# Performance work log

Hardware: AMD Instinct MI355X
Metric: run time of the kernel (lower is better)

Reference implementation:

```python
import jax, jax.numpy as jnp
import numpy as np

V, N, D, H, C = 3, 4096, 512, 128, 5  # views, nodes, in_dim, hidden, classes
NEG = -9.0e15   # mask value from original code (-9000000000000000.0)
NEG_SLOPE = 0.25


def _leaky(x, slope):
    return jnp.where(x >= 0, x, slope * x)


def setup_inputs() -> dict:
    key = jax.random.key(0)
    ks = jax.random.split(key, 24)
    g = lambda i, shape, s=0.05: (jax.random.normal(ks[i], shape, dtype=jnp.float32) * s)
    return {
        "data": jax.random.normal(ks[0], (V, N, D), dtype=jnp.float32),
        "adj": jax.random.randint(ks[1], (V, N, N), 0, 2, dtype=jnp.int32),
        "gac_w": g(2, (V, D, H)), "gac_b": g(3, (V, H)),
        "a1": g(4, (V, H)), "a2": g(5, (V, H)),
        "mlp_w": g(6, (V, D, H)), "mlp_b": g(7, (V, H)),
        "q_w": g(8, (V, H, H)), "q_b": g(9, (V, H)),
        "k_w": g(10, (V, H, H)), "k_b": g(11, (V, H)),
        "v_w": g(12, (V, H, H)), "v_b": g(13, (V, H)),
        "fc_w": g(14, (V, H, H)), "fc_b": g(15, (V, H)),
        "conf_w": g(16, (V, H, 1)), "conf_b": g(17, (V, 1)),
        "mm_w": g(18, (V * H, C)), "mm_b": g(19, (C,)),
    }


def reference(data, adj, gac_w, gac_b, a1, a2, mlp_w, mlp_b,
              q_w, q_b, k_w, k_b, v_w, v_b, fc_w, fc_b,
              conf_w, conf_b, mm_w, mm_b):
    # --- GraphAttentionConv (per view, vectorized over v) ---
    h = jnp.einsum('vnd,vdh->vnh', data, gac_w)               # spmm(input, W)
    e1 = jnp.einsum('vnh,vh->vn', h, a1)                      # h @ a1
    e2 = jnp.einsum('vnh,vh->vn', h, a2)                      # h @ a2
    e = _leaky(e1[:, :, None] + e2[:, None, :], NEG_SLOPE)    # [V,N,N] broadcast-add
    e = jnp.where(adj > 0, e, NEG)                            # mask by dense adjacency
    att = jax.nn.softmax(e, axis=-1)                          # row softmax
    feat = jnp.einsum('vnm,vmh->vnh', att, h) + gac_b[:, None, :]
    feat = _leaky(feat, NEG_SLOPE)                            # F.leaky_relu(GAC out, 0.25)
    # residual MLP branch
    feat = feat + jnp.einsum('vnd,vdh->vnh', data, mlp_w) + mlp_b[:, None, :]

    # --- StructureGuidedFeatureEnhancement (n_heads=1): per-node HxH attention ---
    Q = jnp.einsum('vnh,vho->vno', feat, q_w) + q_b[:, None, :]
    K = jnp.einsum('vnh,vho->vno', feat, k_w) + k_b[:, None, :]
    Vv = jnp.einsum('vnh,vho->vno', feat, v_w) + v_b[:, None, :]
    scale = jnp.sqrt(jnp.asarray(H, jnp.float32))
    A = Q[:, :, :, None] * K[:, :, None, :] / scale           # [V,N,H,H] outer product
    A = jax.nn.softmax(A, axis=-1)
    agg = jnp.einsum('vnio,vno->vni', A, Vv)                  # attention @ V
    agg = jnp.einsum('vnh,vho->vno', agg, fc_w) + fc_b[:, None, :]
    feat = jax.nn.relu(agg)

    # --- TCP confidence gating ---
    conf = jnp.einsum('vnh,vho->vno', feat, conf_w) + conf_b[:, None, :]  # [V,N,1]
    feat = feat * conf

    # --- concat views along feature dim, final classifier ---
    mm = jnp.transpose(feat, (1, 0, 2)).reshape(N, V * H)     # [N, V*H]
    return mm @ mm_w + mm_b                                   # MMlogit [N, C]
```

## Files before the change

### kernel.cpp

```cpp
#include <hip/hip_runtime.h>
#include <hip/hip_bf16.h>

#define V 3
#define N 4096
#define D 512
#define H 128
#define C 5

typedef short short8 __attribute__((ext_vector_type(8)));
typedef float floatx4 __attribute__((ext_vector_type(4)));

__device__ __forceinline__ unsigned short f2bf(float f){
  __hip_bfloat16 h = __float2bfloat16(f);
  return *reinterpret_cast<unsigned short*>(&h);
}

#define TN1 16
__global__ __launch_bounds__(256) void k1_gemm(
    const float* __restrict__ data,
    const float* __restrict__ gac_w,
    const float* __restrict__ mlp_w,
    const float* __restrict__ a1, const float* __restrict__ a2,
    unsigned short* __restrict__ hT, float* __restrict__ mlp_out,
    float* __restrict__ e1, float* __restrict__ e2)
{
  const int v = blockIdx.y;
  const int n0 = blockIdx.x * TN1;
  const int t = threadIdx.x;
  const int half = t >> 7, tt = t & 127;
  __shared__ float ds[D][20];
  __shared__ float epart[2][2][TN1];
  float* comb = &ds[0][0];
  const float* dp = data + ((size_t)v*N + n0)*D;
  for (int j = t; j < TN1*D; j += 256){
    int r = j >> 9, d = j & (D-1);
    ds[d][r] = dp[(size_t)r*D + d];
  }
  __syncthreads();
  float ag[TN1], am[TN1];
  #pragma unroll
  for (int r=0;r<TN1;r++){ ag[r]=0.f; am[r]=0.f; }
  const int d0 = half*256;
  const float* gw = gac_w + (size_t)v*D*H + tt;
  const float* mw = mlp_w + (size_t)v*D*H + tt;
  for (int d=d0; d<d0+256; d++){
    float wg = gw[(size_t)d*H];
    float wm = mw[(size_t)d*H];
    const float4* p = (const float4*)&ds[d][0];
    float4 x0=p[0], x1=p[1], x2=p[2], x3=p[3];
    float xv[16] = {x0.x,x0.y,x0.z,x0.w, x1.x,x1.y,x1.z,x1.w,
                    x2.x,x2.y,x2.z,x2.w, x3.x,x3.y,x3.z,x3.w};
    #pragma unroll
    for (int r=0;r<TN1;r++){
      ag[r] = fmaf(xv[r], wg, ag[r]);
      am[r] = fmaf(xv[r], wm, am[r]);
    }
  }
  __syncthreads();
  if (half == 1){
    #pragma unroll
    for (int r=0;r<TN1;r++){
      comb[r*H + tt]          = ag[r];
      comb[TN1*H + r*H + tt]  = am[r];
    }
  }
  __syncthreads();
  if (half == 0){
    float* mp = mlp_out + ((size_t)v*N + n0)*H + tt;
    unsigned short pk[TN1];
    const float a1v = a1[v*H + tt], a2v = a2[v*H + tt];
    #pragma unroll
    for (int r=0;r<TN1;r++){
      ag[r] += comb[r*H + tt];
      am[r] += comb[TN1*H + r*H + tt];
      mp[(size_t)r*H] = am[r];
      pk[r] = f2bf(ag[r]);
    }
    uint4* hp = (uint4*)(hT + ((size_t)v*H + tt)*N + n0);
    hp[0] = *(uint4*)&pk[0];
    hp[1] = *(uint4*)&pk[8];
    #pragma unroll
    for (int r=0;r<TN1;r++){
      float s1 = ag[r]*a1v, s2 = ag[r]*a2v;
      #pragma unroll
      for (int o=32;o>0;o>>=1){ s1 += __shfl_down(s1,o); s2 += __shfl_down(s2,o); }
      if ((tt&63)==0){ epart[0][tt>>6][r]=s1; epart[1][tt>>6][r]=s2; }
    }
  }
  __syncthreads();
  if (t < TN1)            e1[(size_t)v*N + n0 + t]        = epart[0][0][t]    + epart[0][1][t];
  else if (t < 2*TN1)     e2[(size_t)v*N + n0 + (t-TN1)]  = epart[1][0][t-TN1]+ epart[1][1][t-TN1];
}

#define KC 128
__global__ __launch_bounds__(512) void k2_attn(
    const unsigned short* __restrict__ hT, const int* __restrict__ adj,
    const float* __restrict__ e1g, const float* __restrict__ e2g,
    const float* __restrict__ mlp_out,
    const float* __restrict__ gac_b, const float* __restrict__ mlp_b,
    float* __restrict__ feat)
{
  const int v = blockIdx.y;
  const int n0 = blockIdx.x * 16;
  const int t = threadIdx.x;
  const int w = t >> 6, lane = t & 63;
  __shared__ unsigned short Afrag[4][64][8];
  __shared__ float pden_l[8][16];

  const int pr = t & 15, sm = t >> 4;
  const int p_ks   = sm >> 3;
  const int p_lane = pr + 16*((sm>>1)&3);
  const int p_j0   = 4*(sm&1);
  const float e1r = e1g[(size_t)v*N + n0 + pr];
  const int* aprow = adj + ((size_t)v*N + n0 + pr)*N;
  float psum = 0.f;

  const int col = w*16 + (lane & 15);
  const unsigned short* bcol = hT + ((size_t)v*H + col)*N + ((lane>>4)*8);
  floatx4 acc = {0.f, 0.f, 0.f, 0.f};

  for (int m0 = 0; m0 < N; m0 += KC){
    const float4 e2v = *(const float4*)(e2g + (size_t)v*N + m0 + 4*sm);
    const int4  av  = *(const int4*)(aprow + m0 + 4*sm);
    float e2a[4] = {e2v.x, e2v.y, e2v.z, e2v.w};
    int   aa[4]  = {av.x, av.y, av.z, av.w};
    unsigned int pk[2];
    unsigned short us[4];
    #pragma unroll
    for (int jj=0;jj<4;jj++){
      float x = e1r + e2a[jj];
      x = (x >= 0.f) ? x : 0.25f*x;
      float wv = (aa[jj] > 0) ? __expf(x) : 0.f;
      psum += wv;
      us[jj] = f2bf(wv);
    }
    pk[0] = (unsigned int)us[0] | ((unsigned int)us[1] << 16);
    pk[1] = (unsigned int)us[2] | ((unsigned int)us[3] << 16);
    *(uint2*)&Afrag[p_ks][p_lane][p_j0] = make_uint2(pk[0], pk[1]);
    __syncthreads();
    #pragma unroll
    for (int ks=0; ks<4; ks++){
      short8 a8 = *(const short8*)&Afrag[ks][lane][0];
      short8 b8 = *(const short8*)(bcol + m0 + ks*32);
      acc = __builtin_amdgcn_mfma_f32_16x16x32_bf16(a8, b8, acc, 0, 0, 0);
    }
    __syncthreads();
  }
  psum += __shfl_down(psum, 32);
  psum += __shfl_down(psum, 16);
  if (lane < 16) pden_l[w][lane] = psum;
  __syncthreads();
  const float gb = gac_b[v*H + col];
  const float mb = mlp_b[v*H + col];
  #pragma unroll
  for (int reg=0; reg<4; reg++){
    const int row = (lane>>4)*4 + reg;
    float den = 0.f;
    #pragma unroll
    for (int k=0;k<8;k++) den += pden_l[k][row];
    float x = acc[reg]/den + gb;
    x = (x >= 0.f) ? x : 0.25f*x;
    const size_t idx = ((size_t)v*N + n0 + row)*H + col;
    feat[idx] = x + mlp_out[idx] + mb;
  }
}

#define TN3 8
__global__ __launch_bounds__(128) void k3_sgfe(
    const float* __restrict__ feat,
    const float* __restrict__ qw, const float* __restrict__ qb,
    const float* __restrict__ kw, const float* __restrict__ kb,
    const float* __restrict__ vw, const float* __restrict__ vb,
    const float* __restrict__ fcw, const float* __restrict__ fcb,
    const float* __restrict__ confw, const float* __restrict__ confb,
    float* __restrict__ feat2)
{
  const int v = blockIdx.y;
  const int n0 = blockIdx.x * TN3;
  const int t = threadIdx.x;
  const int W = t >> 6, lane = t & 63;
  __shared__ float fsT[H][12];
  __shared__ float Qs[TN3][H];
  __shared__ float2 KVs[TN3][H];
  __shared__ float As2T[H][12];
  __shared__ float rbuf2[TN3][2];
  const float* fp = feat + ((size_t)v*N + n0)*H + t;
  #pragma unroll
  for (int r=0;r<TN3;r++) fsT[t][r] = fp[(size_t)r*H];
  __syncthreads();
  const float* qwp = qw + (size_t)v*H*H + t;
  const float* kwp = kw + (size_t)v*H*H + t;
  const float* vwp = vw + (size_t)v*H*H + t;
  float Qr[TN3], Kr[TN3], Vr[TN3];
  {
    const float qbv = qb[v*H+t], kbv = kb[v*H+t], vbv = vb[v*H+t];
    #pragma unroll
    for (int r=0;r<TN3;r++){ Qr[r]=qbv; Kr[r]=kbv; Vr[r]=vbv; }
  }
  for (int i=0;i<H;i++){
    float wq = qwp[(size_t)i*H];
    float wk = kwp[(size_t)i*H];
    float wv = vwp[(size_t)i*H];
    float4 f0 = *(const float4*)&fsT[i][0];
    float4 f1 = *(const float4*)&fsT[i][4];
    float fv[8] = {f0.x,f0.y,f0.z,f0.w, f1.x,f1.y,f1.z,f1.w};
    #pragma unroll
    for (int r=0;r<TN3;r++){
      Qr[r] = fmaf(fv[r], wq, Qr[r]);
      Kr[r] = fmaf(fv[r], wk, Kr[r]);
      Vr[r] = fmaf(fv[r], wv, Vr[r]);
    }
  }
  #pragma unroll
  for (int r=0;r<TN3;r++){
    Qs[r][t] = Qr[r];
    KVs[r][t] = make_float2(Kr[r], Vr[r]);
  }
  __syncthreads();
  const float invs = 0.08838834764831845f;
  #pragma unroll
  for (int p=0;p<4;p++){
    const int r = 2*p + W;
    const float qa = Qs[r][lane]   * invs;
    const float qb2 = Qs[r][lane+64] * invs;
    float sA=0.f, aA=0.f, sB=0.f, aB=0.f;
    const float4* kvp = (const float4*)&KVs[r][0];
    #pragma unroll 4
    for (int oo=0; oo<H/2; oo++){
      float4 kv2 = kvp[oo];
      float eA0 = __expf(qa*kv2.x);  sA += eA0; aA = fmaf(eA0, kv2.y, aA);
      float eA1 = __expf(qa*kv2.z);  sA += eA1; aA = fmaf(eA1, kv2.w, aA);
      float eB0 = __expf(qb2*kv2.x); sB += eB0; aB = fmaf(eB0, kv2.y, aB);
      float eB1 = __expf(qb2*kv2.z); sB += eB1; aB = fmaf(eB1, kv2.w, aB);
    }
    As2T[lane][r]    = aA/sA;
    As2T[lane+64][r] = aB/sB;
  }
  __syncthreads();
  const float* fcwp = fcw + (size_t)v*H*H + t;
  const float fcbv = fcb[v*H+t];
  float g[TN3];
  #pragma unroll
  for (int r=0;r<TN3;r++) g[r] = fcbv;
  for (int i=0;i<H;i++){
    float fw = fcwp[(size_t)i*H];
    float4 a0 = *(const float4*)&As2T[i][0];
    float4 a1v = *(const float4*)&As2T[i][4];
    g[0] = fmaf(a0.x, fw, g[0]);  g[1] = fmaf(a0.y, fw, g[1]);
    g[2] = fmaf(a0.z, fw, g[2]);  g[3] = fmaf(a0.w, fw, g[3]);
    g[4] = fmaf(a1v.x, fw, g[4]); g[5] = fmaf(a1v.y, fw, g[5]);
    g[6] = fmaf(a1v.z, fw, g[6]); g[7] = fmaf(a1v.w, fw, g[7]);
  }
  const float cwv = confw[v*H+t];
  const float cbv = confb[v];
  #pragma unroll
  for (int r=0;r<TN3;r++){
    g[r] = fmaxf(g[r], 0.f);
    float psm = g[r]*cwv;
    #pragma unroll
    for (int o=32;o>0;o>>=1) psm += __shfl_down(psm,o);
    if (lane==0) rbuf2[r][W] = psm;
  }
  __syncthreads();
  #pragma unroll
  for (int r=0;r<TN3;r++){
    const float conf = rbuf2[r][0] + rbuf2[r][1] + cbv;
    feat2[((size_t)v*N + n0 + r)*H + t] = g[r]*conf;
  }
}

__global__ __launch_bounds__(64) void k4_cls(
    const float* __restrict__ feat2,
    const float* __restrict__ mm_w, const float* __restrict__ mm_b,
    float* __restrict__ out)
{
  const int n = blockIdx.x, t = threadIdx.x;
  float a[C] = {0,0,0,0,0};
  for (int j=t; j<V*H; j+=64){
    int vv = j >> 7, hh = j & (H-1);
    float f = feat2[((size_t)vv*N + n)*H + hh];
    #pragma unroll
    for (int c=0;c<C;c++) a[c] = fmaf(f, mm_w[j*C+c], a[c]);
  }
  #pragma unroll
  for (int c=0;c<C;c++){
    #pragma unroll
    for (int o=32;o>0;o>>=1) a[c] += __shfl_down(a[c],o);
  }
  if (t==0){
    #pragma unroll
    for (int c=0;c<C;c++) out[(size_t)n*C+c] = a[c] + mm_b[c];
  }
}

extern "C" void kernel_launch(void* const* d_in, const int* in_sizes, int n_in,
                              void* d_out, int out_size, void* d_ws, size_t ws_size,
                              hipStream_t stream)
{
  (void)in_sizes; (void)n_in; (void)out_size; (void)ws_size;
  const float* data  = (const float*)d_in[0];
  const int*   adj   = (const int*)d_in[1];
  const float* gac_w = (const float*)d_in[2];
  const float* gac_b = (const float*)d_in[3];
  const float* a1    = (const float*)d_in[4];
  const float* a2    = (const float*)d_in[5];
  const float* mlp_w = (const float*)d_in[6];
  const float* mlp_b = (const float*)d_in[7];
  const float* q_w   = (const float*)d_in[8];
  const float* q_b   = (const float*)d_in[9];
  const float* k_w   = (const float*)d_in[10];
  const float* k_b   = (const float*)d_in[11];
  const float* v_w   = (const float*)d_in[12];
  const float* v_b   = (const float*)d_in[13];
  const float* fc_w  = (const float*)d_in[14];
  const float* fc_b  = (const float*)d_in[15];
  const float* cw    = (const float*)d_in[16];
  const float* cb    = (const float*)d_in[17];
  const float* mm_w  = (const float*)d_in[18];
  const float* mm_b  = (const float*)d_in[19];

  float* ws = (float*)d_ws;
  const size_t VNH = (size_t)V*N*H;
  float* mlp   = ws;
  float* feat  = ws + VNH;
  float* feat2 = ws + 2*VNH;
  float* e1    = ws + 3*VNH;
  float* e2    = e1 + (size_t)V*N;
  unsigned short* hT = (unsigned short*)(e2 + (size_t)V*N);

  k1_gemm<<<dim3(N/TN1, V), 256, 0, stream>>>(data, gac_w, mlp_w, a1, a2,
                                              hT, mlp, e1, e2);
  k2_attn<<<dim3(N/16, V),  512, 0, stream>>>(hT, adj, e1, e2, mlp, gac_b, mlp_b, feat);
  k3_sgfe<<<dim3(N/TN3, V), 128, 0, stream>>>(feat, q_w, q_b, k_w, k_b, v_w, v_b,
                                              fc_w, fc_b, cw, cb, feat2);
  k4_cls<<<dim3(N),          64, 0, stream>>>(feat2, mm_w, mm_b, (float*)d_out);
}
```

Before: 506.2 us.

## Build attention A-fragments in registers per wave, dropping LDS staging and barriers

The masked-softmax GEMM kernel is restructured so that each wave computes its own bf16 A fragment straight from adj and e2 in registers. It then feeds two MFMA column tiles with that fragment, which removes the shared-memory staging and the two barriers per K chunk. The row denominator comes from a shuffle instead of an LDS reduction, the block shrinks to 256 threads, e1/e2 are pre-scaled by log2(e) so exp2f can replace expf, and bf16 packing is done by hand. In exchange, each of the four waves redundantly reads the same adj rows and recomputes the exponentials, and the hand-written rounding drops NaN handling.

```diff
diff --git a/kernel.cpp b/kernel.cpp
--- a/kernel.cpp
+++ b/kernel.cpp
@@ -6,6 +6,7 @@
 #define D 512
 #define H 128
 #define C 5
+#define LOG2E 1.4426950408889634f
 
 typedef short short8 __attribute__((ext_vector_type(8)));
 typedef float floatx4 __attribute__((ext_vector_type(4)));
@@ -13,6 +14,12 @@
 __device__ __forceinline__ unsigned short f2bf(float f){
   __hip_bfloat16 h = __float2bfloat16(f);
   return *reinterpret_cast<unsigned short*>(&h);
+}
+__device__ __forceinline__ unsigned int pk_bf16(float a, float b){
+  unsigned int ua = __float_as_uint(a), ub = __float_as_uint(b);
+  ua += 0x7FFFu + ((ua >> 16) & 1u);
+  ub += 0x7FFFu + ((ub >> 16) & 1u);
+  return (ua >> 16) | (ub & 0xFFFF0000u);
 }
 
 #define TN1 16
@@ -88,12 +95,11 @@
     }
   }
   __syncthreads();
-  if (t < TN1)            e1[(size_t)v*N + n0 + t]        = epart[0][0][t]    + epart[0][1][t];
-  else if (t < 2*TN1)     e2[(size_t)v*N + n0 + (t-TN1)]  = epart[1][0][t-TN1]+ epart[1][1][t-TN1];
-}
-
-#define KC 128
-__global__ __launch_bounds__(512) void k2_attn(
+  if (t < TN1)        e1[(size_t)v*N + n0 + t]       = LOG2E*(epart[0][0][t]    + epart[0][1][t]);
+  else if (t < 2*TN1) e2[(size_t)v*N + n0 + (t-TN1)] = LOG2E*(epart[1][0][t-TN1]+ epart[1][1][t-TN1]);
+}
+
+__global__ __launch_bounds__(256) void k2_attn(
     const unsigned short* __restrict__ hT, const int* __restrict__ adj,
     const float* __restrict__ e1g, const float* __restrict__ e2g,
     const float* __restrict__ mlp_out,
@@ -102,66 +108,56 @@
 {
   const int v = blockIdx.y;
   const int n0 = blockIdx.x * 16;
-  const int t = threadIdx.x;
-  const int w = t >> 6, lane = t & 63;
-  __shared__ unsigned short Afrag[4][64][8];
-  __shared__ float pden_l[8][16];
-
-  const int pr = t & 15, sm = t >> 4;
-  const int p_ks   = sm >> 3;
-  const int p_lane = pr + 16*((sm>>1)&3);
-  const int p_j0   = 4*(sm&1);
-  const float e1r = e1g[(size_t)v*N + n0 + pr];
-  const int* aprow = adj + ((size_t)v*N + n0 + pr)*N;
+  const int w = threadIdx.x >> 6, lane = threadIdx.x & 63;
+  const int r = lane & 15, quad = lane >> 4;
+  const float e1r = e1g[(size_t)v*N + n0 + r];
+  const int* aprow = adj + ((size_t)v*N + n0 + r)*N + quad*8;
+  const float* e2p = e2g + (size_t)v*N + quad*8;
+  const unsigned short* b0p = hT + ((size_t)v*H + 32*w      + r)*N + quad*8;
+  const unsigned short* b1p = hT + ((size_t)v*H + 32*w + 16 + r)*N + quad*8;
+  floatx4 acc0 = {0.f,0.f,0.f,0.f}, acc1 = {0.f,0.f,0.f,0.f};
   float psum = 0.f;
-
-  const int col = w*16 + (lane & 15);
-  const unsigned short* bcol = hT + ((size_t)v*H + col)*N + ((lane>>4)*8);
-  floatx4 acc = {0.f, 0.f, 0.f, 0.f};
-
-  for (int m0 = 0; m0 < N; m0 += KC){
-    const float4 e2v = *(const float4*)(e2g + (size_t)v*N + m0 + 4*sm);
-    const int4  av  = *(const int4*)(aprow + m0 + 4*sm);
-    float e2a[4] = {e2v.x, e2v.y, e2v.z, e2v.w};
-    int   aa[4]  = {av.x, av.y, av.z, av.w};
-    unsigned int pk[2];
-    unsigned short us[4];
-    #pragma unroll
-    for (int jj=0;jj<4;jj++){
-      float x = e1r + e2a[jj];
-      x = (x >= 0.f) ? x : 0.25f*x;
-      float wv = (aa[jj] > 0) ? __expf(x) : 0.f;
-      psum += wv;
-      us[jj] = f2bf(wv);
-    }
-    pk[0] = (unsigned int)us[0] | ((unsigned int)us[1] << 16);
-    pk[1] = (unsigned int)us[2] | ((unsigned int)us[3] << 16);
-    *(uint2*)&Afrag[p_ks][p_lane][p_j0] = make_uint2(pk[0], pk[1]);
-    __syncthreads();
-    #pragma unroll
-    for (int ks=0; ks<4; ks++){
-      short8 a8 = *(const short8*)&Afrag[ks][lane][0];
-      short8 b8 = *(const short8*)(bcol + m0 + ks*32);
-      acc = __builtin_amdgcn_mfma_f32_16x16x32_bf16(a8, b8, acc, 0, 0, 0);
-    }
-    __syncthreads();
+  #pragma unroll 4
+  for (int k0 = 0; k0 < N; k0 += 32){
+    int4 aa0 = *(const int4*)(aprow + k0);
+    int4 aa1 = *(const int4*)(aprow + k0 + 4);
+    float4 ea = *(const float4*)(e2p + k0);
+    float4 eb = *(const float4*)(e2p + k0 + 4);
+    short8 b8a = *(const short8*)(b0p + k0);
+    short8 b8b = *(const short8*)(b1p + k0);
+    int   am[8] = {aa0.x,aa0.y,aa0.z,aa0.w, aa1.x,aa1.y,aa1.z,aa1.w};
+    float ev[8] = {ea.x,ea.y,ea.z,ea.w, eb.x,eb.y,eb.z,eb.w};
+    float wv[8];
+    #pragma unroll
+    for (int j=0;j<8;j++){
+      float y = e1r + ev[j];
+      y = fmaxf(y, 0.25f*y);
+      float e = exp2f(y);
+      wv[j] = (am[j] > 0) ? e : 0.f;
+      psum += wv[j];
+    }
+    union { short8 s; unsigned int u[4]; } a8;
+    #pragma unroll
+    for (int j=0;j<4;j++) a8.u[j] = pk_bf16(wv[2*j], wv[2*j+1]);
+    acc0 = __builtin_amdgcn_mfma_f32_16x16x32_bf16(a8.s, b8a, acc0, 0, 0, 0);
+    acc1 = __builtin_amdgcn_mfma_f32_16x16x32_bf16(a8.s, b8b, acc1, 0, 0, 0);
   }
   psum += __shfl_down(psum, 32);
   psum += __shfl_down(psum, 16);
-  if (lane < 16) pden_l[w][lane] = psum;
-  __syncthreads();
-  const float gb = gac_b[v*H + col];
-  const float mb = mlp_b[v*H + col];
+  const int col0 = 32*w + r;
+  const float gb0 = gac_b[v*H + col0], gb1 = gac_b[v*H + col0 + 16];
+  const float mb0 = mlp_b[v*H + col0], mb1 = mlp_b[v*H + col0 + 16];
   #pragma unroll
   for (int reg=0; reg<4; reg++){
-    const int row = (lane>>4)*4 + reg;
-    float den = 0.f;
-    #pragma unroll
-    for (int k=0;k<8;k++) den += pden_l[k][row];
-    float x = acc[reg]/den + gb;
-    x = (x >= 0.f) ? x : 0.25f*x;
-    const size_t idx = ((size_t)v*N + n0 + row)*H + col;
-    feat[idx] = x + mlp_out[idx] + mb;
+    const int row = quad*4 + reg;
+    const float den = __shfl(psum, row);
+    const size_t base = ((size_t)v*N + n0 + row)*H;
+    float x0 = acc0[reg]/den + gb0;
+    x0 = (x0 >= 0.f) ? x0 : 0.25f*x0;
+    feat[base + col0] = x0 + mlp_out[base + col0] + mb0;
+    float x1 = acc1[reg]/den + gb1;
+    x1 = (x1 >= 0.f) ? x1 : 0.25f*x1;
+    feat[base + col0 + 16] = x1 + mlp_out[base + col0 + 16] + mb1;
   }
 }
 
@@ -330,7 +326,7 @@
 
   k1_gemm<<<dim3(N/TN1, V), 256, 0, stream>>>(data, gac_w, mlp_w, a1, a2,
                                               hT, mlp, e1, e2);
-  k2_attn<<<dim3(N/16, V),  512, 0, stream>>>(hT, adj, e1, e2, mlp, gac_b, mlp_b, feat);
+  k2_attn<<<dim3(N/16, V),  256, 0, stream>>>(hT, adj, e1, e2, mlp, gac_b, mlp_b, feat);
   k3_sgfe<<<dim3(N/TN3, V), 128, 0, stream>>>(feat, q_w, q_b, k_w, k_b, v_w, v_b,
                                               fc_w, fc_b, cw, cb, feat2);
   k4_cls<<<dim3(N),          64, 0, stream>>>(feat2, mm_w, mm_b, (float*)d_out);
```

Measured after the change: 566.9 us. +12.0%, slower.

## Double-buffer attention weight tiles and prefetch adjacency in graph attention kernel

Applied to the files above, without the earlier changes.

The graph-attention kernel now double-buffers the shared-memory bf16 weight fragments. The next chunk's adjacency and e2 values are loaded and exponentiated while MFMAs run on the current chunk, which removes one barrier per iteration and overlaps global loads with matrix work. e1/e2 are pre-scaled by log2(e) so exp2f can replace __expf, and leaky-relu becomes a fmaxf. Bf16 packing uses a manual round-to-nearest-even bit trick, and unroll pragmas are added to several FMA loops in the other kernels.

```diff
diff --git a/kernel.cpp b/kernel.cpp
--- a/kernel.cpp
+++ b/kernel.cpp
@@ -6,6 +6,7 @@
 #define D 512
 #define H 128
 #define C 5
+#define LOG2E 1.4426950408889634f
 
 typedef short short8 __attribute__((ext_vector_type(8)));
 typedef float floatx4 __attribute__((ext_vector_type(4)));
@@ -13,6 +14,12 @@
 __device__ __forceinline__ unsigned short f2bf(float f){
   __hip_bfloat16 h = __float2bfloat16(f);
   return *reinterpret_cast<unsigned short*>(&h);
+}
+__device__ __forceinline__ unsigned int pk_bf16(float a, float b){
+  unsigned int ua = __float_as_uint(a), ub = __float_as_uint(b);
+  ua += 0x7FFFu + ((ua >> 16) & 1u);
+  ub += 0x7FFFu + ((ub >> 16) & 1u);
+  return (ua >> 16) | (ub & 0xFFFF0000u);
 }
 
 #define TN1 16
@@ -43,6 +50,7 @@
   const int d0 = half*256;
   const float* gw = gac_w + (size_t)v*D*H + tt;
   const float* mw = mlp_w + (size_t)v*D*H + tt;
+  #pragma unroll 4
   for (int d=d0; d<d0+256; d++){
     float wg = gw[(size_t)d*H];
     float wm = mw[(size_t)d*H];
@@ -88,8 +96,8 @@
     }
   }
   __syncthreads();
-  if (t < TN1)            e1[(size_t)v*N + n0 + t]        = epart[0][0][t]    + epart[0][1][t];
-  else if (t < 2*TN1)     e2[(size_t)v*N + n0 + (t-TN1)]  = epart[1][0][t-TN1]+ epart[1][1][t-TN1];
+  if (t < TN1)        e1[(size_t)v*N + n0 + t]       = LOG2E*(epart[0][0][t]    + epart[0][1][t]);
+  else if (t < 2*TN1) e2[(size_t)v*N + n0 + (t-TN1)] = LOG2E*(epart[1][0][t-TN1]+ epart[1][1][t-TN1]);
 }
 
 #define KC 128
@@ -104,7 +112,7 @@
   const int n0 = blockIdx.x * 16;
   const int t = threadIdx.x;
   const int w = t >> 6, lane = t & 63;
-  __shared__ unsigned short Afrag[4][64][8];
+  __shared__ unsigned short Afrag[2][4][64][8];
   __shared__ float pden_l[8][16];
 
   const int pr = t & 15, sm = t >> 4;
@@ -113,36 +121,59 @@
   const int p_j0   = 4*(sm&1);
   const float e1r = e1g[(size_t)v*N + n0 + pr];
   const int* aprow = adj + ((size_t)v*N + n0 + pr)*N;
+  const float* e2row = e2g + (size_t)v*N;
   float psum = 0.f;
 
   const int col = w*16 + (lane & 15);
   const unsigned short* bcol = hT + ((size_t)v*H + col)*N + ((lane>>4)*8);
   floatx4 acc = {0.f, 0.f, 0.f, 0.f};
 
-  for (int m0 = 0; m0 < N; m0 += KC){
-    const float4 e2v = *(const float4*)(e2g + (size_t)v*N + m0 + 4*sm);
-    const int4  av  = *(const int4*)(aprow + m0 + 4*sm);
-    float e2a[4] = {e2v.x, e2v.y, e2v.z, e2v.w};
-    int   aa[4]  = {av.x, av.y, av.z, av.w};
-    unsigned int pk[2];
-    unsigned short us[4];
+  float4 e2v = *(const float4*)(e2row + 4*sm);
+  int4   av  = *(const int4*)(aprow + 4*sm);
+  {
+    float ev[4] = {e2v.x, e2v.y, e2v.z, e2v.w};
+    int   aa[4] = {av.x, av.y, av.z, av.w};
+    float wv[4];
     #pragma unroll
     for (int jj=0;jj<4;jj++){
-      float x = e1r + e2a[jj];
-      x = (x >= 0.f) ? x : 0.25f*x;
-      float wv = (aa[jj] > 0) ? __expf(x) : 0.f;
-      psum += wv;
-      us[jj] = f2bf(wv);
-    }
-    pk[0] = (unsigned int)us[0] | ((unsigned int)us[1] << 16);
-    pk[1] = (unsigned int)us[2] | ((unsigned int)us[3] << 16);
-    *(uint2*)&Afrag[p_ks][p_lane][p_j0] = make_uint2(pk[0], pk[1]);
-    __syncthreads();
+      float y = e1r + ev[jj];
+      y = fmaxf(y, 0.25f*y);
+      float e = exp2f(y);
+      wv[jj] = (aa[jj] > 0) ? e : 0.f;
+      psum += wv[jj];
+    }
+    *(uint2*)&Afrag[0][p_ks][p_lane][p_j0] =
+        make_uint2(pk_bf16(wv[0],wv[1]), pk_bf16(wv[2],wv[3]));
+  }
+  __syncthreads();
+
+  for (int j = 0; j < N/KC; j++){
+    const int cur = j & 1;
+    const int m0 = j * KC;
+    if (j+1 < N/KC){
+      e2v = *(const float4*)(e2row + m0 + KC + 4*sm);
+      av  = *(const int4*)(aprow + m0 + KC + 4*sm);
+    }
     #pragma unroll
     for (int ks=0; ks<4; ks++){
-      short8 a8 = *(const short8*)&Afrag[ks][lane][0];
+      short8 a8 = *(const short8*)&Afrag[cur][ks][lane][0];
       short8 b8 = *(const short8*)(bcol + m0 + ks*32);
       acc = __builtin_amdgcn_mfma_f32_16x16x32_bf16(a8, b8, acc, 0, 0, 0);
+    }
+    if (j+1 < N/KC){
+      float ev[4] = {e2v.x, e2v.y, e2v.z, e2v.w};
+      int   aa[4] = {av.x, av.y, av.z, av.w};
+      float wv[4];
+      #pragma unroll
+      for (int jj=0;jj<4;jj++){
+        float y = e1r + ev[jj];
+        y = fmaxf(y, 0.25f*y);
+        float e = exp2f(y);
+        wv[jj] = (aa[jj] > 0) ? e : 0.f;
+        psum += wv[jj];
+      }
+      *(uint2*)&Afrag[cur^1][p_ks][p_lane][p_j0] =
+          make_uint2(pk_bf16(wv[0],wv[1]), pk_bf16(wv[2],wv[3]));
     }
     __syncthreads();
   }
@@ -197,6 +228,7 @@
     #pragma unroll
     for (int r=0;r<TN3;r++){ Qr[r]=qbv; Kr[r]=kbv; Vr[r]=vbv; }
   }
+  #pragma unroll 2
   for (int i=0;i<H;i++){
     float wq = qwp[(size_t)i*H];
     float wk = kwp[(size_t)i*H];
@@ -242,6 +274,7 @@
   float g[TN3];
   #pragma unroll
   for (int r=0;r<TN3;r++) g[r] = fcbv;
+  #pragma unroll 2
   for (int i=0;i<H;i++){
     float fw = fcwp[(size_t)i*H];
     float4 a0 = *(const float4*)&As2T[i][0];
```

Result: slower. 541.8 us (+7.0%).
